# Kernel tuning notes

Measured on AMD Instinct MI355X. Metric: run time of the kernel, lower is better.

The kernel has to match this reference:

```python
import jax, jax.numpy as jnp
import numpy as np

B, N, C = 2, 2048, 2048
H, KV = 16, 4          # query heads, kv heads
D = C // H             # head_dim = 128
ROPE_BASE = 10000.0


def rope_cos_sin(position_ids, dim):
    # interleaved RoPE: freqs for even indices, repeated pairwise to full dim
    inv_freq = 1.0 / (ROPE_BASE ** (jnp.arange(0, dim, 2, dtype=jnp.float32) / dim))
    ang = position_ids[..., None].astype(jnp.float32) * inv_freq   # [B, N, D/2]
    cos = jnp.repeat(jnp.cos(ang), 2, axis=-1)                     # [B, N, D]
    sin = jnp.repeat(jnp.sin(ang), 2, axis=-1)
    return cos, sin


def rotate_half_interleaved(x):
    # (x0, x1, x2, x3, ...) -> (-x1, x0, -x3, x2, ...)
    x1 = x[..., 0::2]
    x2 = x[..., 1::2]
    return jnp.stack([-x2, x1], axis=-1).reshape(x.shape)


def apply_rotary(x, cos, sin):
    # x: [B, h, N, D]; cos/sin: [B, N, D]
    return x * cos[:, None] + rotate_half_interleaved(x) * sin[:, None]


def setup_inputs() -> dict:
    key = jax.random.key(0)
    ks = jax.random.split(key, 5)
    s = 0.02
    return dict(
        x=jax.random.normal(ks[0], (B, N, C), jnp.float32),
        position_ids=jnp.tile(jnp.arange(N, dtype=jnp.int32), (B, 1)),
        Wq=jax.random.normal(ks[1], (C, C), jnp.float32) * s,
        bq=jnp.zeros((C,), jnp.float32),
        Wk=jax.random.normal(ks[2], (C, KV * D), jnp.float32) * s,
        bk=jnp.zeros((KV * D,), jnp.float32),
        Wv=jax.random.normal(ks[3], (C, KV * D), jnp.float32) * s,
        bv=jnp.zeros((KV * D,), jnp.float32),
        Wo=jax.random.normal(ks[4], (C, C), jnp.float32) * s,
    )


def reference(x, position_ids, Wq, bq, Wk, bk, Wv, bv, Wo):
    Bx, Nx, Cx = x.shape
    q = (x @ Wq + bq).reshape(Bx, Nx, H, D).transpose(0, 2, 1, 3)   # [B,H,N,D]
    k = (x @ Wk + bk).reshape(Bx, Nx, KV, D).transpose(0, 2, 1, 3)  # [B,KV,N,D]
    v = (x @ Wv + bv).reshape(Bx, Nx, KV, D).transpose(0, 2, 1, 3)

    cos, sin = rope_cos_sin(position_ids, D)
    q = apply_rotary(q, cos, sin)
    k = apply_rotary(k, cos, sin)

    # GQA expand: head h uses kv head h // groups (matches unsqueeze+expand+reshape)
    groups = H // KV
    k = jnp.repeat(k, groups, axis=1)   # [B,H,N,D]
    v = jnp.repeat(v, groups, axis=1)

    attn = jnp.einsum('bhqd,bhkd->bhqk', q, k) * (D ** -0.5)        # [B,H,N,N]
    causal_mask = jnp.triu(jnp.ones((Nx, Nx), dtype=bool), 1)
    attn = jnp.where(causal_mask, -jnp.inf, attn)
    attn = jax.nn.softmax(attn, axis=-1)

    out = jnp.einsum('bhqk,bhkd->bhqd', attn, v)
    out = out.transpose(0, 2, 1, 3).reshape(Bx, Nx, Cx)
    return out @ Wo
```

## Files before the change

kernel.cpp:

```cpp
#include <hip/hip_runtime.h>
#include <cstdint>
#include <type_traits>

typedef unsigned short u16;
typedef unsigned int u32;
typedef __bf16 bf16x8 __attribute__((ext_vector_type(8)));
typedef float f32x4 __attribute__((ext_vector_type(4)));

constexpr int BB = 2;
constexpr int SEQ = 2048;
constexpr int CH = 2048;
constexpr int NH = 16;
constexpr int NKV = 4;
constexpr int HD = 128;
constexpr int QKVC = CH + 2 * NKV * HD;

#define DI __device__ __forceinline__

DI u16 f2b(float x) {
  u32 u = __float_as_uint(x);
  u = u + 0x7FFFu + ((u >> 16) & 1u);
  return (u16)(u >> 16);
}
DI float b2f(u16 u) { return __uint_as_float(((u32)u) << 16); }

DI u32 pack2bf(float lo, float hi) {
  return __builtin_amdgcn_perm(__float_as_uint(hi), __float_as_uint(lo), 0x07060302u);
}

DI void glds16(const void* g, void* l) {
  __builtin_amdgcn_global_load_lds(
      (__attribute__((address_space(1))) void*)(uintptr_t)g,
      (__attribute__((address_space(3))) void*)(u32)(uintptr_t)l, 16, 0, 0);
}

__global__ __launch_bounds__(256) void xconv_kernel(const float* __restrict__ in,
                                                    u16* __restrict__ out, int n4) {
  int i = blockIdx.x * 256 + threadIdx.x;
  if (i < n4) {
    float4 v = *(const float4*)&in[(size_t)i * 4];
    ushort4 o;
    o.x = f2b(v.x); o.y = f2b(v.y); o.z = f2b(v.z); o.w = f2b(v.w);
    *(ushort4*)&out[(size_t)i * 4] = o;
  }
}

__global__ __launch_bounds__(256) void wtrans4_kernel(
    const float* __restrict__ Wq, const float* __restrict__ Wk,
    const float* __restrict__ Wv, const float* __restrict__ Wo,
    u16* __restrict__ wqkvt, u16* __restrict__ wot) {
  const int z = blockIdx.z;
  const float* in;
  u16* out;
  int Cc;
  if (z == 0)      { in = Wq; out = wqkvt;                                Cc = CH; }
  else if (z == 1) { in = Wk; out = wqkvt + (size_t)CH * CH;              Cc = NKV * HD; }
  else if (z == 2) { in = Wv; out = wqkvt + (size_t)(CH + NKV * HD) * CH; Cc = NKV * HD; }
  else             { in = Wo; out = wot;                                  Cc = CH; }
  if ((int)blockIdx.y * 64 >= Cc) return;

  __shared__ u16 tile[64 * 65];
  const int r0 = blockIdx.x * 64, c0 = blockIdx.y * 64;
  const int tid = threadIdx.x;
  for (int c = tid; c < 1024; c += 256) {
    int r = c >> 4, col = (c & 15) * 4;
    float4 v = *(const float4*)&in[(size_t)(r0 + r) * Cc + c0 + col];
    tile[r * 65 + col + 0] = f2b(v.x);
    tile[r * 65 + col + 1] = f2b(v.y);
    tile[r * 65 + col + 2] = f2b(v.z);
    tile[r * 65 + col + 3] = f2b(v.w);
  }
  __syncthreads();
  for (int c = tid; c < 1024; c += 256) {
    int r = c >> 4, col = (c & 15) * 4;
    ushort4 v;
    v.x = tile[(col + 0) * 65 + r];
    v.y = tile[(col + 1) * 65 + r];
    v.z = tile[(col + 2) * 65 + r];
    v.w = tile[(col + 3) * 65 + r];
    *(ushort4*)&out[(size_t)(c0 + r) * CH + r0 + col] = v;
  }
}

__global__ __launch_bounds__(256) void vtrans_kernel(const u16* __restrict__ in,
                                                     u16* __restrict__ out) {
  __shared__ u16 tile[64 * 65];
  const int s = blockIdx.z, n0 = blockIdx.x * 64, d0 = blockIdx.y * 64;
  const int tid = threadIdx.x;
  const u16* ip = in + (size_t)s * SEQ * HD + (size_t)n0 * HD + d0;
  u16* op = out + (size_t)s * HD * SEQ + (size_t)d0 * SEQ + n0;
  for (int c = tid; c < 1024; c += 256) {
    int r = c >> 4, col = (c & 15) * 4;
    ushort4 v = *(const ushort4*)&ip[(size_t)r * HD + col];
    tile[r * 65 + col + 0] = v.x;
    tile[r * 65 + col + 1] = v.y;
    tile[r * 65 + col + 2] = v.z;
    tile[r * 65 + col + 3] = v.w;
  }
  __syncthreads();
  for (int c = tid; c < 1024; c += 256) {
    int r = c >> 4, col = (c & 15) * 4;
    ushort4 v;
    v.x = tile[(col + 0) * 65 + r];
    v.y = tile[(col + 1) * 65 + r];
    v.z = tile[(col + 2) * 65 + r];
    v.w = tile[(col + 3) * 65 + r];
    int u = col;
    int w = (u & 3) | (((u >> 5) & 1) << 2) | (((u >> 2) & 3) << 3) | (((u >> 4) & 1) << 5);
    int glp = (w >> 3) ^ (r & 7);
    int colp = glp * 8 + (w & 7);
    *(ushort4*)&op[(size_t)r * SEQ + colp] = v;
  }
}

template <int MODE>
__global__ __launch_bounds__(256, 3) void gemm_kernel(
    const u16* __restrict__ A, const u16* __restrict__ Bt,
    u16* __restrict__ Cb, float* __restrict__ Cf, u16* __restrict__ Vn,
    const float* __restrict__ bq, const float* __restrict__ bk,
    const float* __restrict__ bv, int M, int Nn, int K) {
  __shared__ u16 As[128 * 64];
  __shared__ u16 Bs[128 * 64];
  const int tid = threadIdx.x;
  const int lane = tid & 63, wave = tid >> 6;
  const int wrow = wave >> 1, wcol = wave & 1;
  const int m0 = blockIdx.x * 128, n0 = blockIdx.y * 128;
  const int lm = lane & 15, lq = lane >> 4;
  f32x4 acc[4][4] = {};

  const int grow = tid >> 3;
  const int gcol = ((lane & 7) ^ (lane >> 3)) * 8;
  const u16* ag = A + (size_t)(m0 + grow) * K + gcol;
  const u16* bg = Bt + (size_t)(n0 + grow) * K + gcol;
  char* asb = (char*)As + wave * 1024;
  char* bsb = (char*)Bs + wave * 1024;
  const size_t rowskip = (size_t)32 * K;

  for (int k = 0; k < K; k += 64) {
    __syncthreads();
#pragma unroll
    for (int c = 0; c < 4; c++) {
      glds16(ag + c * rowskip + k, asb + c * 4096);
      glds16(bg + c * rowskip + k, bsb + c * 4096);
    }
    __syncthreads();
#pragma unroll
    for (int kk = 0; kk < 2; kk++) {
      bf16x8 af[4], bfr[4];
      const int slot = ((kk * 4 + lq) ^ (lm & 7)) * 16;
#pragma unroll
      for (int i = 0; i < 4; i++)
        af[i] = *(const bf16x8*)((const char*)As + (wrow * 64 + i * 16 + lm) * 128 + slot);
#pragma unroll
      for (int j = 0; j < 4; j++)
        bfr[j] = *(const bf16x8*)((const char*)Bs + (wcol * 64 + j * 16 + lm) * 128 + slot);
#pragma unroll
      for (int i = 0; i < 4; i++)
#pragma unroll
        for (int j = 0; j < 4; j++)
          acc[i][j] = __builtin_amdgcn_mfma_f32_16x16x32_bf16(af[i], bfr[j], acc[i][j], 0, 0, 0);
    }
  }

#pragma unroll
  for (int i = 0; i < 4; i++) {
    const int mg = m0 + wrow * 64 + i * 16 + lq * 4;
#pragma unroll
    for (int j = 0; j < 4; j++) {
      const int ng = n0 + wcol * 64 + j * 16 + lm;
      float bias = 0.f;
      if (MODE == 0)
        bias = (ng < CH) ? bq[ng] : (ng < CH + NKV * HD ? bk[ng - CH] : bv[ng - CH - NKV * HD]);
#pragma unroll
      for (int r = 0; r < 4; r++) {
        float v = acc[i][j][r] + bias;
        if (MODE == 0) {
          if (ng >= CH + NKV * HD) {
            int tok = mg + r;
            int bidx = tok >> 11, n = tok & (SEQ - 1);
            int vcol = ng - (CH + NKV * HD);
            int kh = vcol >> 7, d = vcol & (HD - 1);
            Vn[((size_t)(bidx * NKV + kh) * SEQ + n) * HD + d] = f2b(v);
          } else {
            Cb[(size_t)(mg + r) * Nn + ng] = f2b(v);
          }
        } else {
          Cf[(size_t)(mg + r) * Nn + ng] = v;
        }
      }
    }
  }
}

__global__ __launch_bounds__(256) void rope_kernel(
    const u16* __restrict__ qkv, const int* __restrict__ pos,
    u16* __restrict__ Qo, u16* __restrict__ Ko) {
  __shared__ float cs_s[64], sn_s[64];
  const int tok = blockIdx.x;
  const int b = tok >> 11, n = tok & (SEQ - 1);
  const int t = threadIdx.x;
  const u16* row = qkv + (size_t)tok * QKVC;
  const float LN1E4_64 = 0.14391156831212788f;

  if (t < 64) {
    float ang = (float)pos[tok] * expf(-(float)t * LN1E4_64);
    float sn, cs;
    sincosf(ang, &sn, &cs);
    cs_s[t] = cs;
    sn_s[t] = sn;
  }
  __syncthreads();

  for (int idx = t; idx < NH * 64; idx += 256) {
    int hh = idx >> 6, i = idx & 63;
    float cs = cs_s[i], sn = sn_s[i];
    float q0v = b2f(row[hh * 128 + 2 * i]);
    float q1v = b2f(row[hh * 128 + 2 * i + 1]);
    size_t off = ((size_t)(b * NH + hh) * SEQ + n) * HD + 2 * i;
    Qo[off] = f2b(q0v * cs - q1v * sn);
    Qo[off + 1] = f2b(q1v * cs + q0v * sn);
  }
  {
    int kh = t >> 6, i = t & 63;
    float cs = cs_s[i], sn = sn_s[i];
    float k0v = b2f(row[CH + kh * 128 + 2 * i]);
    float k1v = b2f(row[CH + kh * 128 + 2 * i + 1]);
    int d0 = 2 * i;
    int g = d0 >> 3;
    int gp = (g & 8) | ((g ^ n) & 7);
    int dp = gp * 8 + (d0 & 7);
    size_t off = ((size_t)(b * NKV + kh) * SEQ + n) * HD + dp;
    Ko[off] = f2b(k0v * cs - k1v * sn);
    Ko[off + 1] = f2b(k1v * cs + k0v * sn);
  }
}

__global__ __launch_bounds__(256, 2) void flash_kernel(
    const u16* __restrict__ Q, const u16* __restrict__ Kk,
    const u16* __restrict__ Vt, u16* __restrict__ Oo) {
  __shared__ u16 Kb[2][64 * 128];
  __shared__ u16 Vb[2][144 * 64];
  const int tid = threadIdx.x, lane = tid & 63, wave = tid >> 6;
  const int lm = lane & 15, lq = lane >> 4;
  const int p = blockIdx.x;
  const int h = blockIdx.y, b = blockIdx.z;
  const int q0A = p * 64, q0B = (31 - p) * 64;
  const int kvh = h >> 2;
  const u16* Qg = Q + (size_t)(b * NH + h) * SEQ * HD;
  const u16* Kg = Kk + (size_t)(b * NKV + kvh) * SEQ * HD;
  const u16* Vg = Vt + (size_t)(b * NKV + kvh) * HD * SEQ;

  if (tid < 128) Vb[tid >> 6][128 * 64 + (tid & 63)] = 0x3F80;

  bf16x8 qf[2][4];
#pragma unroll
  for (int qg = 0; qg < 2; qg++) {
    const int q0g = qg ? q0B : q0A;
    const u16* qrow = Qg + (size_t)(q0g + wave * 16 + lm) * HD;
#pragma unroll
    for (int kd = 0; kd < 4; kd++)
      qf[qg][kd] = *(const bf16x8*)&qrow[kd * 32 + lq * 8];
  }

  f32x4 oacc[2][8] = {};
  f32x4 oaccS[2] = {};
  const float SCL2 = 0.12754325f;
  const int nIter = 32 - p;

  auto stage = [&](int kv0, int bufi) {
    const char* kb = (const char*)(Kg + (size_t)kv0 * HD);
    char* kl = (char*)&Kb[bufi][0];
    const char* vbb = (const char*)(Vg + (size_t)kv0);
    char* vl = (char*)&Vb[bufi][0];
#pragma unroll
    for (int c = 0; c < 4; c++) {
      int ch = wave * 4 + c;
      glds16(kb + ch * 1024 + lane * 16, kl + ch * 1024);
      glds16(vbb + (size_t)(ch * 8 + (lane >> 3)) * (SEQ * 2) + (lane & 7) * 16,
             vl + ch * 1024);
    }
  };

  stage(0, 0);

  for (int t = 0; t < nIter; t++) {
    __syncthreads();
    if (t + 1 < nIter) stage((t + 1) * 64, (t + 1) & 1);
    const u16* Ks = &Kb[t & 1][0];
    const u16* Vs = &Vb[t & 1][0];
    const int kv0 = t * 64;
    const bool actA = (t <= p);

    auto run = [&](auto dualc) {
      constexpr bool DUAL = decltype(dualc)::value;
      f32x4 sv[2][4] = {};
#pragma unroll
      for (int nt = 0; nt < 4; nt++)
#pragma unroll
        for (int kd = 0; kd < 4; kd++) {
          int g = kd * 4 + lq;
          int gpp = (g & 8) | ((g ^ lm) & 7);
          bf16x8 kf = *(const bf16x8*)&Ks[(nt * 16 + lm) * 128 + gpp * 8];
          sv[1][nt] = __builtin_amdgcn_mfma_f32_16x16x32_bf16(kf, qf[1][kd], sv[1][nt], 0, 0, 0);
          if constexpr (DUAL)
            sv[0][nt] = __builtin_amdgcn_mfma_f32_16x16x32_bf16(kf, qf[0][kd], sv[0][nt], 0, 0, 0);
        }

      alignas(16) u32 pad[2][2][4];
      auto softmax = [&](int qg, int q0g) {
        const int base = q0g + wave * 16;
        if (kv0 + 63 > base) {
          const int qrow = base + lm;
#pragma unroll
          for (int nt = 0; nt < 4; nt++) {
            float pv[4];
#pragma unroll
            for (int r = 0; r < 4; r++) {
              int kvg = kv0 + nt * 16 + lq * 4 + r;
              float e = exp2f(sv[qg][nt][r] * SCL2);
              pv[r] = (kvg > qrow) ? 0.f : e;
            }
            pad[qg][nt & 1][(nt >> 1) * 2 + 0] = pack2bf(pv[0], pv[1]);
            pad[qg][nt & 1][(nt >> 1) * 2 + 1] = pack2bf(pv[2], pv[3]);
          }
        } else {
#pragma unroll
          for (int nt = 0; nt < 4; nt++) {
            float pv[4];
#pragma unroll
            for (int r = 0; r < 4; r++) pv[r] = exp2f(sv[qg][nt][r] * SCL2);
            pad[qg][nt & 1][(nt >> 1) * 2 + 0] = pack2bf(pv[0], pv[1]);
            pad[qg][nt & 1][(nt >> 1) * 2 + 1] = pack2bf(pv[2], pv[3]);
          }
        }
      };
      softmax(1, q0B);
      if constexpr (DUAL) softmax(0, q0A);

#pragma unroll
      for (int ks = 0; ks < 2; ks++) {
        const int glp = (ks * 4 + lq) ^ (lm & 7);
        const bf16x8 pa1 = *(const bf16x8*)&pad[1][ks][0];
        const bf16x8 pa0 = *(const bf16x8*)&pad[0][ks][0];
#pragma unroll
        for (int dt = 0; dt < 8; dt++) {
          bf16x8 vf = *(const bf16x8*)&Vs[(dt * 16 + lm) * 64 + glp * 8];
          oacc[1][dt] = __builtin_amdgcn_mfma_f32_16x16x32_bf16(pa1, vf, oacc[1][dt], 0, 0, 0);
          if constexpr (DUAL)
            oacc[0][dt] = __builtin_amdgcn_mfma_f32_16x16x32_bf16(pa0, vf, oacc[0][dt], 0, 0, 0);
        }
        bf16x8 vf8 = *(const bf16x8*)&Vs[(128 + lm) * 64 + glp * 8];
        oaccS[1] = __builtin_amdgcn_mfma_f32_16x16x32_bf16(pa1, vf8, oaccS[1], 0, 0, 0);
        if constexpr (DUAL)
          oaccS[0] = __builtin_amdgcn_mfma_f32_16x16x32_bf16(pa0, vf8, oaccS[0], 0, 0, 0);
      }
    };
    if (actA) run(std::integral_constant<bool, true>{});
    else      run(std::integral_constant<bool, false>{});
  }

  u16* orow = Oo + (size_t)b * SEQ * CH + (size_t)h * HD;
#pragma unroll
  for (int qg = 0; qg < 2; qg++) {
    const int q0g = qg ? q0B : q0A;
    float inv[4];
#pragma unroll
    for (int r = 0; r < 4; r++) inv[r] = 1.0f / __shfl(oaccS[qg][r], lq * 16);
    const int qrow_base = q0g + wave * 16 + lq * 4;
#pragma unroll
    for (int dt = 0; dt < 8; dt++)
#pragma unroll
      for (int r = 0; r < 4; r++)
        orow[(size_t)(qrow_base + r) * CH + dt * 16 + lm] = f2b(oacc[qg][dt][r] * inv[r]);
  }
}

extern "C" void kernel_launch(void* const* d_in, const int* in_sizes, int n_in,
                              void* d_out, int out_size, void* d_ws, size_t ws_size,
                              hipStream_t stream) {
  const float* x = (const float*)d_in[0];
  const int* pos = (const int*)d_in[1];
  const float* Wq = (const float*)d_in[2];
  const float* bq = (const float*)d_in[3];
  const float* Wk = (const float*)d_in[4];
  const float* bk = (const float*)d_in[5];
  const float* Wv = (const float*)d_in[6];
  const float* bv = (const float*)d_in[7];
  const float* Wo = (const float*)d_in[8];
  float* out = (float*)d_out;

  char* ws = (char*)d_ws;
  u16* xb = (u16*)ws;    ws += (size_t)BB * SEQ * CH * 2;
  u16* wqkvt = (u16*)ws; ws += (size_t)QKVC * CH * 2;
  u16* wot = (u16*)ws;   ws += (size_t)CH * CH * 2;
  u16* qkv = (u16*)ws;   ws += (size_t)BB * SEQ * QKVC * 2;
  u16* qr = (u16*)ws;    ws += (size_t)BB * NH * SEQ * HD * 2;
  u16* kr = (u16*)ws;    ws += (size_t)BB * NKV * SEQ * HD * 2;
  u16* vn = (u16*)ws;    ws += (size_t)BB * NKV * SEQ * HD * 2;
  u16* vt = (u16*)ws;    ws += (size_t)BB * NKV * SEQ * HD * 2;
  u16* ao = (u16*)ws;    ws += (size_t)BB * SEQ * CH * 2;

  xconv_kernel<<<dim3(BB * SEQ * CH / 1024), 256, 0, stream>>>(x, xb, BB * SEQ * CH / 4);
  wtrans4_kernel<<<dim3(32, 32, 4), 256, 0, stream>>>(Wq, Wk, Wv, Wo, wqkvt, wot);
  gemm_kernel<0><<<dim3(32, 24), 256, 0, stream>>>(xb, wqkvt, qkv, (float*)nullptr, vn,
                                                   bq, bk, bv, BB * SEQ, QKVC, CH);
  rope_kernel<<<dim3(BB * SEQ), 256, 0, stream>>>(qkv, pos, qr, kr);
  vtrans_kernel<<<dim3(SEQ / 64, HD / 64, BB * NKV), 256, 0, stream>>>(vn, vt);
  flash_kernel<<<dim3(16, NH, BB), 256, 0, stream>>>(qr, kr, vt, ao);
  gemm_kernel<1><<<dim3(32, 16), 256, 0, stream>>>(ao, wot, (u16*)nullptr, out, nullptr,
                                                   nullptr, nullptr, nullptr, BB * SEQ, CH, CH);
}
```

Baseline: 311.0 us.

## Replace GEMM with double-buffered 256-wide tile kernel using 512 threads

Rewrites the QKV and output-projection GEMMs to use larger tiles (256x256 for QKV, 128x256 for output) with 8 waves, dynamic shared memory and double-buffered LDS staging. Global loads for the next K tile are issued while MFMAs run on the current one, with explicit barriers, waitcnts and priority hints, so load latency overlaps compute and operand reuse per block goes up. In exchange the grids are smaller (192 and 256 blocks), which may underfill a 256-CU device, and register pressure is higher.

```diff
diff --git a/kernel.cpp b/kernel.cpp
--- a/kernel.cpp
+++ b/kernel.cpp
@@ -114,57 +114,97 @@
 }
 
 template <int MODE>
-__global__ __launch_bounds__(256, 3) void gemm_kernel(
+__global__ __launch_bounds__(512, 2) void gemm256_kernel(
     const u16* __restrict__ A, const u16* __restrict__ Bt,
     u16* __restrict__ Cb, float* __restrict__ Cf, u16* __restrict__ Vn,
     const float* __restrict__ bq, const float* __restrict__ bk,
     const float* __restrict__ bv, int M, int Nn, int K) {
-  __shared__ u16 As[128 * 64];
-  __shared__ u16 Bs[128 * 64];
+  constexpr int BM = (MODE == 0) ? 256 : 128;
+  constexpr int MI = BM / 32;
+  constexpr int NPH = MI / 2;
+  extern __shared__ char smem[];
+  u16* As = (u16*)smem;
+  u16* Bs = As + 2 * BM * 64;
+
   const int tid = threadIdx.x;
   const int lane = tid & 63, wave = tid >> 6;
-  const int wrow = wave >> 1, wcol = wave & 1;
-  const int m0 = blockIdx.x * 128, n0 = blockIdx.y * 128;
+  const int wrow = wave >> 2, wcol = wave & 3;
   const int lm = lane & 15, lq = lane >> 4;
-  f32x4 acc[4][4] = {};
-
-  const int grow = tid >> 3;
-  const int gcol = ((lane & 7) ^ (lane >> 3)) * 8;
-  const u16* ag = A + (size_t)(m0 + grow) * K + gcol;
-  const u16* bg = Bt + (size_t)(n0 + grow) * K + gcol;
-  char* asb = (char*)As + wave * 1024;
-  char* bsb = (char*)Bs + wave * 1024;
-  const size_t rowskip = (size_t)32 * K;
-
-  for (int k = 0; k < K; k += 64) {
-    __syncthreads();
-#pragma unroll
-    for (int c = 0; c < 4; c++) {
-      glds16(ag + c * rowskip + k, asb + c * 4096);
-      glds16(bg + c * rowskip + k, bsb + c * 4096);
+  const int m0 = blockIdx.x * BM, n0 = blockIdx.y * 256;
+  const int srow = tid >> 3;
+  const int sswz = (tid & 7) ^ (srow & 7);
+
+  f32x4 acc[MI][4] = {};
+
+  auto stageA = [&](int kt, int b) {
+#pragma unroll
+    for (int s = 0; s < BM / 64; s++)
+      glds16(A + (size_t)(m0 + s * 64 + srow) * K + kt + sswz * 8,
+             (char*)As + b * (BM * 128) + (s * 64 + wave * 8) * 128);
+  };
+  auto stageB = [&](int kt, int b) {
+#pragma unroll
+    for (int s = 0; s < 4; s++)
+      glds16(Bt + (size_t)(n0 + s * 64 + srow) * K + kt + sswz * 8,
+             (char*)Bs + b * (256 * 128) + (s * 64 + wave * 8) * 128);
+  };
+
+  const int NT = K >> 6;
+  stageA(0, 0);
+  stageB(0, 0);
+  asm volatile("s_waitcnt vmcnt(0)" ::: "memory");
+  __builtin_amdgcn_s_barrier();
+
+  for (int T = 0; T < NT; T++) {
+    const int buf = T & 1;
+    const u16* Asb = As + buf * (BM * 64);
+    const u16* Bsb = Bs + buf * (256 * 64);
+    const int kt1 = (T + 1) << 6;
+    const bool pf = (T + 1 < NT);
+    bf16x8 bfv[4][2];
+#pragma unroll
+    for (int q = 0; q < NPH; q++) {
+      bf16x8 af[2][2];
+#pragma unroll
+      for (int ii = 0; ii < 2; ii++)
+#pragma unroll
+        for (int kk = 0; kk < 2; kk++)
+          af[ii][kk] = *(const bf16x8*)&Asb[(wrow * (BM / 2) + (q * 2 + ii) * 16 + lm) * 64 +
+                                            (((kk * 4 + lq) ^ (lm & 7)) * 8)];
+      if (q == 0) {
+#pragma unroll
+        for (int j = 0; j < 4; j++)
+#pragma unroll
+          for (int kk = 0; kk < 2; kk++)
+            bfv[j][kk] = *(const bf16x8*)&Bsb[(wcol * 64 + j * 16 + lm) * 64 +
+                                              (((kk * 4 + lq) ^ (lm & 7)) * 8)];
+        if (pf) {
+          stageA(kt1, buf ^ 1);
+          if (NPH == 2) stageB(kt1, buf ^ 1);
+        }
+      }
+      if (NPH == 4 && q == 1 && pf) stageB(kt1, buf ^ 1);
+      __builtin_amdgcn_s_barrier();
+      asm volatile("s_waitcnt lgkmcnt(0)" ::: "memory");
+      __builtin_amdgcn_sched_barrier(0);
+      __builtin_amdgcn_s_setprio(1);
+#pragma unroll
+      for (int ii = 0; ii < 2; ii++)
+#pragma unroll
+        for (int j = 0; j < 4; j++)
+#pragma unroll
+          for (int kk = 0; kk < 2; kk++)
+            acc[q * 2 + ii][j] = __builtin_amdgcn_mfma_f32_16x16x32_bf16(
+                af[ii][kk], bfv[j][kk], acc[q * 2 + ii][j], 0, 0, 0);
+      __builtin_amdgcn_s_setprio(0);
+      if (q == NPH - 1) asm volatile("s_waitcnt vmcnt(0)" ::: "memory");
+      __builtin_amdgcn_s_barrier();
     }
-    __syncthreads();
-#pragma unroll
-    for (int kk = 0; kk < 2; kk++) {
-      bf16x8 af[4], bfr[4];
-      const int slot = ((kk * 4 + lq) ^ (lm & 7)) * 16;
-#pragma unroll
-      for (int i = 0; i < 4; i++)
-        af[i] = *(const bf16x8*)((const char*)As + (wrow * 64 + i * 16 + lm) * 128 + slot);
-#pragma unroll
-      for (int j = 0; j < 4; j++)
-        bfr[j] = *(const bf16x8*)((const char*)Bs + (wcol * 64 + j * 16 + lm) * 128 + slot);
-#pragma unroll
-      for (int i = 0; i < 4; i++)
-#pragma unroll
-        for (int j = 0; j < 4; j++)
-          acc[i][j] = __builtin_amdgcn_mfma_f32_16x16x32_bf16(af[i], bfr[j], acc[i][j], 0, 0, 0);
-    }
-  }
-
-#pragma unroll
-  for (int i = 0; i < 4; i++) {
-    const int mg = m0 + wrow * 64 + i * 16 + lq * 4;
+  }
+
+#pragma unroll
+  for (int i = 0; i < MI; i++) {
+    const int mg = m0 + wrow * (BM / 2) + i * 16 + lq * 4;
 #pragma unroll
     for (int j = 0; j < 4; j++) {
       const int ng = n0 + wcol * 64 + j * 16 + lm;
@@ -400,13 +440,22 @@
   u16* vt = (u16*)ws;    ws += (size_t)BB * NKV * SEQ * HD * 2;
   u16* ao = (u16*)ws;    ws += (size_t)BB * SEQ * CH * 2;
 
+  static int attr_done = 0;
+  if (!attr_done) {
+    hipFuncSetAttribute(reinterpret_cast<const void*>(gemm256_kernel<0>),
+                        hipFuncAttributeMaxDynamicSharedMemorySize, 131072);
+    hipFuncSetAttribute(reinterpret_cast<const void*>(gemm256_kernel<1>),
+                        hipFuncAttributeMaxDynamicSharedMemorySize, 131072);
+    attr_done = 1;
+  }
+
   xconv_kernel<<<dim3(BB * SEQ * CH / 1024), 256, 0, stream>>>(x, xb, BB * SEQ * CH / 4);
   wtrans4_kernel<<<dim3(32, 32, 4), 256, 0, stream>>>(Wq, Wk, Wv, Wo, wqkvt, wot);
-  gemm_kernel<0><<<dim3(32, 24), 256, 0, stream>>>(xb, wqkvt, qkv, (float*)nullptr, vn,
-                                                   bq, bk, bv, BB * SEQ, QKVC, CH);
+  gemm256_kernel<0><<<dim3(16, 12), 512, 131072, stream>>>(xb, wqkvt, qkv, (float*)nullptr,
+                                                           vn, bq, bk, bv, BB * SEQ, QKVC, CH);
   rope_kernel<<<dim3(BB * SEQ), 256, 0, stream>>>(qkv, pos, qr, kr);
   vtrans_kernel<<<dim3(SEQ / 64, HD / 64, BB * NKV), 256, 0, stream>>>(vn, vt);
   flash_kernel<<<dim3(16, NH, BB), 256, 0, stream>>>(qr, kr, vt, ao);
-  gemm_kernel<1><<<dim3(32, 16), 256, 0, stream>>>(ao, wot, (u16*)nullptr, out, nullptr,
-                                                   nullptr, nullptr, nullptr, BB * SEQ, CH, CH);
-}
+  gemm256_kernel<1><<<dim3(32, 8), 512, 98304, stream>>>(ao, wot, (u16*)nullptr, out, nullptr,
+                                                         nullptr, nullptr, nullptr, BB * SEQ, CH, CH);
+}
```

Result: no change. 305.2 us (-1.9%).
